# Optimization experiments

Hardware: AMD Instinct MI355X
Metric: run time of the kernel (lower is better)

The kernel has to match this reference:

```python
import jax, jax.numpy as jnp
import numpy as np

DIM = 192
STATE = 64
B = 8
H = 64
W = 64
EPS_LN = 1e-5
EPS_BN = 1e-5


def _layernorm(x, g, b):
    m = jnp.mean(x, axis=-1, keepdims=True)
    v = jnp.mean((x - m) ** 2, axis=-1, keepdims=True)
    return (x - m) / jnp.sqrt(v + EPS_LN) * g + b


def _linear(x, w, b=None):
    # torch Linear convention: w is [out, in]
    y = jnp.einsum('...i,oi->...o', x, w)
    return y if b is None else y + b


def _parallel_scan(A, Bd, xp):
    # A, Bd, xp: [B, L, S]; h_t = A_t*h_{t-1} + Bd_t*xp_t via log-space cumsum
    A_safe = jnp.clip(A, 0.001, 0.999)
    log_A = jnp.log(A_safe + 1e-10)
    log_cum_A = jnp.cumsum(log_A, axis=1)
    log_cum_A_max = jnp.max(log_cum_A, axis=1, keepdims=True)
    cum_A = jnp.exp(log_cum_A - log_cum_A_max)
    BX = Bd * xp
    # prepend zeros, drop last: normalizer uses cumprod up to t-1
    log_pad = jnp.pad(log_cum_A - log_cum_A_max, ((0, 0), (1, 0), (0, 0)))[:, :-1]
    BX_norm = BX * jnp.exp(-log_pad)
    return jnp.cumsum(BX_norm, axis=1) * cum_A


def _ssm(x, ln_g, ln_b, xp_w, xp_b, dt_w, dt_b, A_log, B_w, C_w, Dp, out_w, out_b):
    xn = _layernorm(x, ln_g, ln_b)
    delta = jax.nn.softplus(_linear(xn, dt_w, dt_b)) * 0.01 + 0.0001  # [B,L,S]
    B_t = _linear(xn, B_w)
    C_t = _linear(xn, C_w)
    A = -jnp.exp(A_log)  # [S]
    x_proj = _linear(xn, xp_w, xp_b)
    deltaA = jnp.clip(delta * A, -10.0, -0.0001)
    A_disc = jnp.exp(deltaA)
    B_disc = delta * B_t
    h = _parallel_scan(A_disc, B_disc, x_proj)
    y = C_t * h
    y = jnp.where(jnp.all(jnp.isfinite(y)), y, jnp.zeros_like(y))
    y = _linear(y, out_w, out_b)
    return y + jnp.clip(Dp, -2.0, 2.0) * x


def reference(x, ln1_g, ln1_b, ln2_g, ln2_b, dw_w, bn_g, bn_b, bn_rm, bn_rv,
              ssm_ln_g, ssm_ln_b, xp_w, xp_b, dt_w, dt_b, A_log, B_w, C_w,
              D_param, out_w, out_b, mlp_w1, mlp_b1, mlp_w2, mlp_b2,
              alpha_local, alpha_ssm, alpha_mlp):
    identity = x
    # depthwise 3x3 conv + BatchNorm2d (eval mode, running stats)
    xc = jax.lax.conv_general_dilated(
        x, dw_w, (1, 1), 'SAME', feature_group_count=DIM,
        dimension_numbers=('NCHW', 'OIHW', 'NCHW'))
    scale = (bn_g / jnp.sqrt(bn_rv + EPS_BN))[None, :, None, None]
    x_local = (xc - bn_rm[None, :, None, None]) * scale + bn_b[None, :, None, None]
    # SSM branch on flattened spatial sequence
    x_seq = x.transpose(0, 2, 3, 1).reshape(B, H * W, DIM)
    x_seq = _layernorm(x_seq, ln1_g, ln1_b)
    x_seq = _ssm(x_seq, ssm_ln_g, ssm_ln_b, xp_w, xp_b, dt_w, dt_b, A_log,
                 B_w, C_w, D_param, out_w, out_b)
    x_ssm = x_seq.reshape(B, H, W, DIM).transpose(0, 3, 1, 2)
    xr = identity + alpha_local * x_local + alpha_ssm * x_ssm
    # residual MLP (dropout = identity at inference)
    x_mlp = xr.transpose(0, 2, 3, 1).reshape(B, H * W, DIM)
    x_mlp = _layernorm(x_mlp, ln2_g, ln2_b)
    x_mlp = _linear(jax.nn.gelu(_linear(x_mlp, mlp_w1, mlp_b1), approximate=False),
                    mlp_w2, mlp_b2)
    return xr + alpha_mlp * x_mlp.reshape(B, H, W, DIM).transpose(0, 3, 1, 2)


def setup_inputs() -> dict:
    key = jax.random.key(0)
    ks = jax.random.split(key, 12)
    def nrm(k, shape, s):
        return jax.random.normal(k, shape, jnp.float32) * s
    f32 = jnp.float32
    return {
        'x': jax.random.normal(ks[0], (B, DIM, H, W), f32),
        'ln1_g': jnp.ones(DIM, f32), 'ln1_b': jnp.zeros(DIM, f32),
        'ln2_g': jnp.ones(DIM, f32), 'ln2_b': jnp.zeros(DIM, f32),
        'dw_w': nrm(ks[1], (DIM, 1, 3, 3), 0.2),
        'bn_g': jnp.ones(DIM, f32), 'bn_b': jnp.zeros(DIM, f32),
        'bn_rm': jnp.zeros(DIM, f32), 'bn_rv': jnp.ones(DIM, f32),
        'ssm_ln_g': jnp.ones(DIM, f32), 'ssm_ln_b': jnp.zeros(DIM, f32),
        'xp_w': nrm(ks[2], (STATE, DIM), 0.05), 'xp_b': jnp.zeros(STATE, f32),
        'dt_w': nrm(ks[3], (STATE, DIM), 0.05), 'dt_b': jnp.zeros(STATE, f32),
        'A_log': jnp.log(jax.random.uniform(ks[4], (STATE,), f32) * 0.8 + 0.2),
        'B_w': nrm(ks[5], (STATE, DIM), 0.05),
        'C_w': nrm(ks[6], (STATE, DIM), 0.05),
        'D_param': jnp.zeros(DIM, f32),
        'out_w': nrm(ks[7], (DIM, STATE), 0.05), 'out_b': jnp.zeros(DIM, f32),
        'mlp_w1': nrm(ks[8], (4 * DIM, DIM), 0.03), 'mlp_b1': jnp.zeros(4 * DIM, f32),
        'mlp_w2': nrm(ks[9], (DIM, 4 * DIM), 0.03), 'mlp_b2': jnp.zeros(DIM, f32),
        'alpha_local': jnp.full((1,), 0.5, f32),
        'alpha_ssm': jnp.full((1,), 0.5, f32),
        'alpha_mlp': jnp.full((1,), 0.5, f32),
    }
```

## Files before the change

kernel.cpp:

```cpp
#include <hip/hip_runtime.h>
#include <hip/hip_bf16.h>
#include <math.h>


#define DEV static __device__ __forceinline__

constexpr int Bn = 8, Dm = 192, Ln = 4096, Sn = 64, Hd = 768;

typedef __attribute__((ext_vector_type(8))) short bf16x8;
typedef __attribute__((ext_vector_type(4))) float f32x4;

DEV float wave_sum(float v) {
#pragma unroll
  for (int off = 1; off < 64; off <<= 1) v += __shfl_xor(v, off);
  return v;
}

DEV short f2b(float x) {
  __hip_bfloat16 h = __float2bfloat16(x);
  return *(short*)&h;
}

DEV float b2f(short x) {
  __hip_bfloat16 h = *(__hip_bfloat16*)&x;
  return __bfloat162float(h);
}

__global__ __launch_bounds__(256) void k_ln(
    const float* __restrict__ x, const float* __restrict__ g1, const float* __restrict__ b1,
    const float* __restrict__ g2, const float* __restrict__ b2,
    short* __restrict__ xnb, short* __restrict__ xln1b) {
  __shared__ __align__(16) float tile[Dm * 65];
  int b = blockIdx.y, l0 = blockIdx.x * 64, tid = threadIdx.x;
  const float* xb = x + (size_t)b * Dm * Ln;
  for (int i = tid; i < Dm * 16; i += 256) {
    int d = i >> 4, l4 = (i & 15) << 2;
    float4 v = *(const float4*)&xb[d * Ln + l0 + l4];
    tile[d * 65 + l4]     = v.x; tile[d * 65 + l4 + 1] = v.y;
    tile[d * 65 + l4 + 2] = v.z; tile[d * 65 + l4 + 3] = v.w;
  }
  __syncthreads();
  int lane = tid & 63, wv = tid >> 6;
  float ga0 = g1[lane], ga1 = g1[lane + 64], ga2 = g1[lane + 128];
  float bb0 = b1[lane], bb1 = b1[lane + 64], bb2 = b1[lane + 128];
  float gc0 = g2[lane], gc1 = g2[lane + 64], gc2 = g2[lane + 128];
  float bc0 = b2[lane], bc1 = b2[lane + 64], bc2 = b2[lane + 128];
  for (int li = wv; li < 64; li += 4) {
    float v0 = tile[lane * 65 + li], v1 = tile[(lane + 64) * 65 + li], v2 = tile[(lane + 128) * 65 + li];
    float s  = wave_sum(v0 + v1 + v2);
    float sq = wave_sum(v0 * v0 + v1 * v1 + v2 * v2);
    float m = s * (1.f / 192.f);
    float inv = rsqrtf(sq * (1.f / 192.f) - m * m + 1e-5f);
    float y0 = (v0 - m) * inv * ga0 + bb0;
    float y1 = (v1 - m) * inv * ga1 + bb1;
    float y2 = (v2 - m) * inv * ga2 + bb2;
    float s2  = wave_sum(y0 + y1 + y2);
    float sq2 = wave_sum(y0 * y0 + y1 * y1 + y2 * y2);
    float m2 = s2 * (1.f / 192.f);
    float inv2 = rsqrtf(sq2 * (1.f / 192.f) - m2 * m2 + 1e-5f);
    size_t base = ((size_t)b * Ln + l0 + li) * Dm;
    xln1b[base + lane]       = f2b(y0);
    xln1b[base + lane + 64]  = f2b(y1);
    xln1b[base + lane + 128] = f2b(y2);
    xnb[base + lane]       = f2b((y0 - m2) * inv2 * gc0 + bc0);
    xnb[base + lane + 64]  = f2b((y1 - m2) * inv2 * gc1 + bc1);
    xnb[base + lane + 128] = f2b((y2 - m2) * inv2 * gc2 + bc2);
  }
}

__global__ __launch_bounds__(256) void k_wconv(
    const float* __restrict__ dt_w, const float* __restrict__ B_w,
    const float* __restrict__ C_w, const float* __restrict__ xp_w,
    const float* __restrict__ out_w, const float* __restrict__ w1,
    const float* __restrict__ w2, short* __restrict__ wb) {
  int i = blockIdx.x * 256 + threadIdx.x;
  const float4* src;
  if (i < 3072)       src = (const float4*)dt_w + i;
  else if (i < 6144)  src = (const float4*)B_w + (i - 3072);
  else if (i < 9216)  src = (const float4*)C_w + (i - 6144);
  else if (i < 12288) src = (const float4*)xp_w + (i - 9216);
  else if (i < 15360) src = (const float4*)out_w + (i - 12288);
  else if (i < 52224) src = (const float4*)w1 + (i - 15360);
  else                src = (const float4*)w2 + (i - 52224);
  float4 v = *src;
  int o = i * 4;
  wb[o]     = f2b(v.x); wb[o + 1] = f2b(v.y);
  wb[o + 2] = f2b(v.z); wb[o + 3] = f2b(v.w);
}

__global__ __launch_bounds__(256) void k_proj(
    const short* __restrict__ xnb, const short* __restrict__ wcat,
    const float* __restrict__ dt_b, const float* __restrict__ xp_b,
    const float* __restrict__ A_log, float* __restrict__ abc) {
  __shared__ __align__(16) short As[64 * 72];
  __shared__ __align__(16) short Bs[256 * 72];
  int m0 = blockIdx.x * 64, tid = threadIdx.x;
  int lane = tid & 63, l16 = lane & 15, quad = lane >> 4, w = tid >> 6;
  f32x4 acc[16] = {};
  for (int kt = 0; kt < 3; kt++) {
    int kb = kt * 64;
    for (int i = tid; i < 512; i += 256) {
      int row = i >> 3, c8 = (i & 7) * 8;
      *(float4*)&As[row * 72 + c8] = *(const float4*)&xnb[(size_t)(m0 + row) * 192 + kb + c8];
    }
    for (int i = tid; i < 2048; i += 256) {
      int row = i >> 3, c8 = (i & 7) * 8;
      *(float4*)&Bs[row * 72 + c8] = *(const float4*)&wcat[(size_t)row * 192 + kb + c8];
    }
    __syncthreads();
#pragma unroll
    for (int ks = 0; ks < 2; ks++) {
      int ko = ks * 32 + quad * 8;
      bf16x8 a0 = *(const bf16x8*)&As[(w * 16 + l16) * 72 + ko];
#pragma unroll
      for (int nh = 0; nh < 2; nh++) {
        bf16x8 bfr[8];
#pragma unroll
        for (int j = 0; j < 8; j++) bfr[j] = *(const bf16x8*)&Bs[((nh * 8 + j) * 16 + l16) * 72 + ko];
#pragma unroll
        for (int j = 0; j < 8; j++)
          acc[nh * 8 + j] = __builtin_amdgcn_mfma_f32_16x16x32_bf16(a0, bfr[j], acc[nh * 8 + j], 0, 0, 0);
      }
    }
    __syncthreads();
  }
  float Av[4], dtb[4], xpb[4];
#pragma unroll
  for (int ni = 0; ni < 4; ni++) {
    int s = ni * 16 + l16;
    Av[ni] = -expf(A_log[s]); dtb[ni] = dt_b[s]; xpb[ni] = xp_b[s];
  }
#pragma unroll
  for (int r = 0; r < 4; r++) {
    int m = m0 + w * 16 + quad * 4 + r;
    float* orow = abc + (size_t)m * 192;
#pragma unroll
    for (int ni = 0; ni < 4; ni++) {
      int s = ni * 16 + l16;
      float z = acc[ni][r] + dtb[ni];
      float sp = (z > 20.f) ? z : log1pf(expf(z));
      float delta = sp * 0.01f + 0.0001f;
      float bt  = acc[ni + 4][r];
      float ct  = acc[ni + 8][r];
      float xpv = acc[ni + 12][r] + xpb[ni];
      float dA = fminf(fmaxf(delta * Av[ni], -10.f), -0.0001f);
      float Ae = fminf(fmaxf(expf(dA), 0.001f), 0.999f) + 1e-10f;
      orow[s]       = Ae;
      orow[64 + s]  = delta * bt * xpv;
      orow[128 + s] = ct;
    }
  }
}

__global__ __launch_bounds__(64) void k_scan1(const float* __restrict__ abc, float* __restrict__ sums) {
  int c = blockIdx.x, b = blockIdx.y, s = threadIdx.x;
  const float* p = abc + ((size_t)b * Ln + c * 32) * 192;
  float prodA = 1.f, h = 0.f;
  int t = 0;
  if (c == 0) { prodA = p[s]; h = p[64 + s]; t = 1; }
#pragma unroll 4
  for (; t < 32; t++) {
    float a = p[t * 192 + s], bx = p[t * 192 + 64 + s];
    h = a * (h + bx);
    prodA *= a;
  }
  int ci = b * 128 + c;
  sums[(ci * 2 + 0) * 64 + s] = prodA;
  sums[(ci * 2 + 1) * 64 + s] = h;
}

__global__ __launch_bounds__(64) void k_scan2(const float* __restrict__ sums, float* __restrict__ carries) {
  int b = blockIdx.x, s = threadIdx.x;
  float cur = 0.f;
#pragma unroll 4
  for (int c = 0; c < 128; c++) {
    int ci = b * 128 + c;
    carries[ci * 64 + s] = cur;
    cur = sums[(ci * 2 + 0) * 64 + s] * cur + sums[(ci * 2 + 1) * 64 + s];
  }
}

__global__ __launch_bounds__(64) void k_scan3(const float* __restrict__ abc, const float* __restrict__ carries,
                                              short* __restrict__ y) {
  int c = blockIdx.x, b = blockIdx.y, s = threadIdx.x;
  size_t r0 = (size_t)b * Ln + c * 32;
  const float* p = abc + r0 * 192;
  short* yo = y + r0 * 64;
  float h = carries[(b * 128 + c) * 64 + s];
  int t = 0;
  if (c == 0) { h = p[64 + s]; yo[s] = f2b(p[128 + s] * h); t = 1; }
#pragma unroll 4
  for (; t < 32; t++) {
    float a = p[t * 192 + s], bx = p[t * 192 + 64 + s], ct = p[t * 192 + 128 + s];
    h = a * (h + bx);
    yo[t * 64 + s] = f2b(ct * h);
  }
}

__global__ __launch_bounds__(256) void k_out(
    const short* __restrict__ y, const short* __restrict__ owb, const float* __restrict__ out_b,
    const float* __restrict__ Dp, const short* __restrict__ xln1b, float* __restrict__ sout) {
  __shared__ __align__(16) short As[96 * 72];
  __shared__ __align__(16) short Bs[64 * 72];
  int l0g = blockIdx.x * 64, d0 = blockIdx.y * 96, tid = threadIdx.x;
  int lane = tid & 63, l16 = lane & 15, quad = lane >> 4;
  int wm = (tid >> 6) >> 1, wn = (tid >> 6) & 1;
  f32x4 acc[3][2] = {};
  for (int i = tid; i < 768; i += 256) {
    int row = i >> 3, c8 = (i & 7) * 8;
    *(float4*)&As[row * 72 + c8] = *(const float4*)&owb[(d0 + row) * 64 + c8];
  }
  for (int i = tid; i < 512; i += 256) {
    int row = i >> 3, c8 = (i & 7) * 8;
    *(float4*)&Bs[row * 72 + c8] = *(const float4*)&y[(size_t)(l0g + row) * 64 + c8];
  }
  __syncthreads();
#pragma unroll
  for (int ks = 0; ks < 2; ks++) {
    int ko = ks * 32 + quad * 8;
    bf16x8 a[3], b[2];
#pragma unroll
    for (int mi = 0; mi < 3; mi++) a[mi] = *(const bf16x8*)&As[(wm * 48 + mi * 16 + l16) * 72 + ko];
#pragma unroll
    for (int ni = 0; ni < 2; ni++) b[ni] = *(const bf16x8*)&Bs[(wn * 32 + ni * 16 + l16) * 72 + ko];
#pragma unroll
    for (int mi = 0; mi < 3; mi++)
#pragma unroll
      for (int ni = 0; ni < 2; ni++)
        acc[mi][ni] = __builtin_amdgcn_mfma_f32_16x16x32_bf16(a[mi], b[ni], acc[mi][ni], 0, 0, 0);
  }
  int bb = l0g >> 12;
#pragma unroll
  for (int mi = 0; mi < 3; mi++)
#pragma unroll
    for (int r = 0; r < 4; r++) {
      int d = d0 + wm * 48 + mi * 16 + quad * 4 + r;
      float ob = out_b[d];
      float dc = fminf(fmaxf(Dp[d], -2.f), 2.f);
#pragma unroll
      for (int ni = 0; ni < 2; ni++) {
        int l = l0g + wn * 32 + ni * 16 + l16;
        float v = acc[mi][ni][r] + ob;
        if (dc != 0.f) v += dc * b2f(xln1b[(size_t)l * 192 + d]);
        sout[((size_t)bb * Dm + d) * Ln + (l & 4095)] = v;
      }
    }
}

__global__ __launch_bounds__(256) void k_conv(
    const float* __restrict__ x, const float* __restrict__ dw,
    const float* __restrict__ bn_g, const float* __restrict__ bn_b,
    const float* __restrict__ bn_rm, const float* __restrict__ bn_rv,
    const float* __restrict__ sout, const float* __restrict__ a_loc,
    const float* __restrict__ a_ssm, float* __restrict__ xr) {
  __shared__ __align__(16) float xs[64 * 64];
  int d = blockIdx.x, b = blockIdx.y, tid = threadIdx.x;
  const float* xp = x + ((size_t)b * Dm + d) * Ln;
  for (int i = tid; i < 1024; i += 256) ((float4*)xs)[i] = ((const float4*)xp)[i];
  __syncthreads();
  float w[9];
#pragma unroll
  for (int k = 0; k < 9; k++) w[k] = dw[d * 9 + k];
  float scale = bn_g[d] * rsqrtf(bn_rv[d] + 1e-5f);
  float rm = bn_rm[d], bb = bn_b[d];
  float al = a_loc[0], as_ = a_ssm[0];
  const float* sp = sout + ((size_t)b * Dm + d) * Ln;
  float* xo = xr + ((size_t)b * Dm + d) * Ln;
  for (int i = tid; i < 4096; i += 256) {
    int h = i >> 6, wc = i & 63;
    float acc = 0.f;
#pragma unroll
    for (int kh = 0; kh < 3; kh++) {
      int hh = h + kh - 1;
      if (hh < 0 || hh >= 64) continue;
#pragma unroll
      for (int kw = 0; kw < 3; kw++) {
        int ww2 = wc + kw - 1;
        if (ww2 < 0 || ww2 >= 64) continue;
        acc += xs[hh * 64 + ww2] * w[kh * 3 + kw];
      }
    }
    float xl = (acc - rm) * scale + bb;
    xo[i] = xs[i] + al * xl + as_ * sp[i];
  }
}

__global__ __launch_bounds__(256) void k_ln2(
    const float* __restrict__ xr, const float* __restrict__ g, const float* __restrict__ bb,
    short* __restrict__ xn2) {
  __shared__ __align__(16) float tile[Dm * 65];
  int b = blockIdx.y, l0 = blockIdx.x * 64, tid = threadIdx.x;
  const float* xb = xr + (size_t)b * Dm * Ln;
  for (int i = tid; i < Dm * 16; i += 256) {
    int d = i >> 4, l4 = (i & 15) << 2;
    float4 v = *(const float4*)&xb[d * Ln + l0 + l4];
    tile[d * 65 + l4]     = v.x; tile[d * 65 + l4 + 1] = v.y;
    tile[d * 65 + l4 + 2] = v.z; tile[d * 65 + l4 + 3] = v.w;
  }
  __syncthreads();
  int lane = tid & 63, wv = tid >> 6;
  float g0 = g[lane], g1v = g[lane + 64], g2v = g[lane + 128];
  float b0 = bb[lane], b1v = bb[lane + 64], b2v = bb[lane + 128];
  for (int li = wv; li < 64; li += 4) {
    float v0 = tile[lane * 65 + li], v1 = tile[(lane + 64) * 65 + li], v2 = tile[(lane + 128) * 65 + li];
    float s  = wave_sum(v0 + v1 + v2);
    float sq = wave_sum(v0 * v0 + v1 * v1 + v2 * v2);
    float m = s * (1.f / 192.f);
    float inv = rsqrtf(sq * (1.f / 192.f) - m * m + 1e-5f);
    size_t base = ((size_t)b * Ln + l0 + li) * Dm;
    xn2[base + lane]       = f2b((v0 - m) * inv * g0 + b0);
    xn2[base + lane + 64]  = f2b((v1 - m) * inv * g1v + b1v);
    xn2[base + lane + 128] = f2b((v2 - m) * inv * g2v + b2v);
  }
}

__global__ __launch_bounds__(256) void k_gemm1(
    const short* __restrict__ xn2, const short* __restrict__ w1b,
    const float* __restrict__ b1h, short* __restrict__ hid) {
  __shared__ __align__(16) short smem[2 * 128 * 88];
  short* As = smem;
  short* Bs = smem + 128 * 88;
  int m0 = blockIdx.x * 128, n0 = blockIdx.y * 128, tid = threadIdx.x;
  int lane = tid & 63, l16 = lane & 15, quad = lane >> 4;
  int wm = (tid >> 6) >> 1, wn = (tid >> 6) & 1;
  f32x4 acc[4][4] = {};
  for (int kt = 0; kt < 3; kt++) {
    int kb = kt * 64;
    for (int i = tid; i < 1024; i += 256) {
      int row = i >> 3, c8 = (i & 7) * 8;
      *(float4*)&As[row * 88 + c8] = *(const float4*)&xn2[(size_t)(m0 + row) * 192 + kb + c8];
      *(float4*)&Bs[row * 88 + c8] = *(const float4*)&w1b[(size_t)(n0 + row) * 192 + kb + c8];
    }
    __syncthreads();
#pragma unroll
    for (int ks = 0; ks < 2; ks++) {
      int ko = ks * 32 + quad * 8;
      bf16x8 a[4], b[4];
#pragma unroll
      for (int mi = 0; mi < 4; mi++) a[mi] = *(const bf16x8*)&As[(wm * 64 + mi * 16 + l16) * 88 + ko];
#pragma unroll
      for (int ni = 0; ni < 4; ni++) b[ni] = *(const bf16x8*)&Bs[(wn * 64 + ni * 16 + l16) * 88 + ko];
#pragma unroll
      for (int mi = 0; mi < 4; mi++)
#pragma unroll
        for (int ni = 0; ni < 4; ni++)
          acc[mi][ni] = __builtin_amdgcn_mfma_f32_16x16x32_bf16(a[mi], b[ni], acc[mi][ni], 0, 0, 0);
    }
    __syncthreads();
  }
  short* Cs = smem;
  float bias4[4];
#pragma unroll
  for (int ni = 0; ni < 4; ni++) bias4[ni] = b1h[n0 + wn * 64 + ni * 16 + l16];
#pragma unroll
  for (int mi = 0; mi < 4; mi++)
#pragma unroll
    for (int ni = 0; ni < 4; ni++) {
      int n = wn * 64 + ni * 16 + l16;
#pragma unroll
      for (int r = 0; r < 4; r++) {
        int m = wm * 64 + mi * 16 + quad * 4 + r;
        float v = acc[mi][ni][r] + bias4[ni];
        float g = 0.5f * v * (1.f + erff(v * 0.70710678118f));
        Cs[m * 136 + n] = f2b(g);
      }
    }
  __syncthreads();
  for (int i = tid; i < 2048; i += 256) {
    int m = i >> 4, ch = i & 15;
    *(float4*)&hid[(size_t)(m0 + m) * 768 + n0 + ch * 8] = *(const float4*)&Cs[m * 136 + ch * 8];
  }
}

__global__ __launch_bounds__(256) void k_gemm2(
    const short* __restrict__ hid, const short* __restrict__ w2b,
    const float* __restrict__ b2o, const float* __restrict__ xr,
    const float* __restrict__ am, float* __restrict__ out) {
  __shared__ __align__(16) short Wt[96 * 88];
  __shared__ __align__(16) short Ht[64 * 88];
  int l0g = blockIdx.x * 64, d0 = blockIdx.y * 96, tid = threadIdx.x;
  int lane = tid & 63, l16 = lane & 15, quad = lane >> 4;
  int wm = (tid >> 6) >> 1, wn = (tid >> 6) & 1;
  f32x4 acc[3][2] = {};
  for (int kt = 0; kt < 12; kt++) {
    int kb = kt * 64;
    for (int i = tid; i < 768; i += 256) {
      int row = i >> 3, c8 = (i & 7) * 8;
      *(float4*)&Wt[row * 88 + c8] = *(const float4*)&w2b[(size_t)(d0 + row) * 768 + kb + c8];
    }
    for (int i = tid; i < 512; i += 256) {
      int row = i >> 3, c8 = (i & 7) * 8;
      *(float4*)&Ht[row * 88 + c8] = *(const float4*)&hid[(size_t)(l0g + row) * 768 + kb + c8];
    }
    __syncthreads();
#pragma unroll
    for (int ks = 0; ks < 2; ks++) {
      int ko = ks * 32 + quad * 8;
      bf16x8 a[3], b[2];
#pragma unroll
      for (int mi = 0; mi < 3; mi++) a[mi] = *(const bf16x8*)&Wt[(wm * 48 + mi * 16 + l16) * 88 + ko];
#pragma unroll
      for (int ni = 0; ni < 2; ni++) b[ni] = *(const bf16x8*)&Ht[(wn * 32 + ni * 16 + l16) * 88 + ko];
#pragma unroll
      for (int mi = 0; mi < 3; mi++)
#pragma unroll
        for (int ni = 0; ni < 2; ni++)
          acc[mi][ni] = __builtin_amdgcn_mfma_f32_16x16x32_bf16(a[mi], b[ni], acc[mi][ni], 0, 0, 0);
    }
    __syncthreads();
  }
  float alpha = am[0];
#pragma unroll
  for (int mi = 0; mi < 3; mi++)
#pragma unroll
    for (int r = 0; r < 4; r++) {
      int d = d0 + wm * 48 + mi * 16 + quad * 4 + r;
      float bias = b2o[d];
#pragma unroll
      for (int ni = 0; ni < 2; ni++) {
        int lg = l0g + wn * 32 + ni * 16 + l16;
        size_t idx = ((size_t)(lg >> 12) * Dm + d) * Ln + (lg & 4095);
        out[idx] = xr[idx] + alpha * (acc[mi][ni][r] + bias);
      }
    }
}

extern "C" void kernel_launch(void* const* d_in, const int* in_sizes, int n_in,
                              void* d_out, int out_size, void* d_ws, size_t ws_size,
                              hipStream_t stream) {
  (void)in_sizes; (void)n_in; (void)out_size; (void)ws_size;
  const float* x     = (const float*)d_in[0];
  const float* ln1_g = (const float*)d_in[1];
  const float* ln1_b = (const float*)d_in[2];
  const float* ln2_g = (const float*)d_in[3];
  const float* ln2_b = (const float*)d_in[4];
  const float* dw_w  = (const float*)d_in[5];
  const float* bn_g  = (const float*)d_in[6];
  const float* bn_b  = (const float*)d_in[7];
  const float* bn_rm = (const float*)d_in[8];
  const float* bn_rv = (const float*)d_in[9];
  const float* ssm_g = (const float*)d_in[10];
  const float* ssm_b = (const float*)d_in[11];
  const float* xp_w  = (const float*)d_in[12];
  const float* xp_b  = (const float*)d_in[13];
  const float* dt_w  = (const float*)d_in[14];
  const float* dt_b  = (const float*)d_in[15];
  const float* A_log = (const float*)d_in[16];
  const float* B_w   = (const float*)d_in[17];
  const float* C_w   = (const float*)d_in[18];
  const float* Dp    = (const float*)d_in[19];
  const float* out_w = (const float*)d_in[20];
  const float* out_b = (const float*)d_in[21];
  const float* w1    = (const float*)d_in[22];
  const float* b1    = (const float*)d_in[23];
  const float* w2    = (const float*)d_in[24];
  const float* b2    = (const float*)d_in[25];
  const float* a_loc = (const float*)d_in[26];
  const float* a_ssm = (const float*)d_in[27];
  const float* a_mlp = (const float*)d_in[28];

  float* ws = (float*)d_ws;
  short* xnb   = (short*)ws;
  short* xln1b = (short*)(ws + 3145728);
  float* abc   = ws + 6291456;
  short* yB    = (short*)(ws + 12582912);
  float* sout  = ws + 13729792;
  float* xr    = ws + 20021248;
  short* wb    = (short*)(ws + 26312704);
  float* sums  = ws + 26490880;
  float* carr  = ws + 26621952;
  short* wcatb = wb;
  short* owb   = wb + 49152;
  short* w1b   = wb + 61440;
  short* w2b   = wb + 208896;
  short* xn2   = (short*)ws;
  short* hid   = (short*)(ws + 6291456);
  float* out   = (float*)d_out;

  k_ln   <<<dim3(64, 8),  256, 0, stream>>>(x, ln1_g, ln1_b, ssm_g, ssm_b, xnb, xln1b);
  k_wconv<<<dim3(348),    256, 0, stream>>>(dt_w, B_w, C_w, xp_w, out_w, w1, w2, wb);
  k_proj <<<dim3(512),    256, 0, stream>>>(xnb, wcatb, dt_b, xp_b, A_log, abc);
  k_scan1<<<dim3(128, 8),  64, 0, stream>>>(abc, sums);
  k_scan2<<<dim3(8),       64, 0, stream>>>(sums, carr);
  k_scan3<<<dim3(128, 8),  64, 0, stream>>>(abc, carr, yB);
  k_out  <<<dim3(512, 2), 256, 0, stream>>>(yB, owb, out_b, Dp, xln1b, sout);
  k_conv <<<dim3(192, 8), 256, 0, stream>>>(x, dw_w, bn_g, bn_b, bn_rm, bn_rv, sout, a_loc, a_ssm, xr);
  k_ln2  <<<dim3(64, 8),  256, 0, stream>>>(xr, ln2_g, ln2_b, xn2);
  k_gemm1<<<dim3(256, 6), 256, 0, stream>>>(xn2, w1b, b1, hid);
  k_gemm2<<<dim3(512, 2), 256, 0, stream>>>(hid, w2b, b2, xr, a_mlp, out);
}
```

Before: 294.8 us.

## Fuse weight conversion into layernorm kernel and pack scan inputs as bf16

Merges the weight-to-bf16 conversion into the layernorm kernel as an extra grid row, removing one launch. Splits the interleaved fp32 A/BX/C scan buffer into a fp32 A array and a packed pair of bf16 BX and C values, cutting the scan's read traffic from 12 to 8 bytes per element. This lowers the precision of BX and C used in the recurrence, which adds some rounding error. The workspace layout is also reshuffled so the xn2 and hid buffers no longer alias earlier ones.

```diff
diff --git a/kernel.cpp b/kernel.cpp
--- a/kernel.cpp
+++ b/kernel.cpp
@@ -26,12 +26,33 @@
   return __bfloat162float(h);
 }
 
-__global__ __launch_bounds__(256) void k_ln(
+__global__ __launch_bounds__(256) void k_prep(
     const float* __restrict__ x, const float* __restrict__ g1, const float* __restrict__ b1,
     const float* __restrict__ g2, const float* __restrict__ b2,
-    short* __restrict__ xnb, short* __restrict__ xln1b) {
+    short* __restrict__ xnb, short* __restrict__ xln1b,
+    const float* __restrict__ dt_w, const float* __restrict__ B_w,
+    const float* __restrict__ C_w, const float* __restrict__ xp_w,
+    const float* __restrict__ out_w, const float* __restrict__ w1,
+    const float* __restrict__ w2, short* __restrict__ wb) {
   __shared__ __align__(16) float tile[Dm * 65];
-  int b = blockIdx.y, l0 = blockIdx.x * 64, tid = threadIdx.x;
+  int tid = threadIdx.x;
+  if (blockIdx.y == 8) {
+    for (int i = blockIdx.x * 256 + tid; i < 89088; i += 64 * 256) {
+      const float4* src;
+      if (i < 3072)       src = (const float4*)dt_w + i;
+      else if (i < 6144)  src = (const float4*)B_w + (i - 3072);
+      else if (i < 9216)  src = (const float4*)C_w + (i - 6144);
+      else if (i < 12288) src = (const float4*)xp_w + (i - 9216);
+      else if (i < 15360) src = (const float4*)out_w + (i - 12288);
+      else if (i < 52224) src = (const float4*)w1 + (i - 15360);
+      else                src = (const float4*)w2 + (i - 52224);
+      float4 v = *src;
+      int o = i * 4;
+      wb[o] = f2b(v.x); wb[o + 1] = f2b(v.y); wb[o + 2] = f2b(v.z); wb[o + 3] = f2b(v.w);
+    }
+    return;
+  }
+  int b = blockIdx.y, l0 = blockIdx.x * 64;
   const float* xb = x + (size_t)b * Dm * Ln;
   for (int i = tid; i < Dm * 16; i += 256) {
     int d = i >> 4, l4 = (i & 15) << 2;
@@ -68,30 +89,10 @@
   }
 }
 
-__global__ __launch_bounds__(256) void k_wconv(
-    const float* __restrict__ dt_w, const float* __restrict__ B_w,
-    const float* __restrict__ C_w, const float* __restrict__ xp_w,
-    const float* __restrict__ out_w, const float* __restrict__ w1,
-    const float* __restrict__ w2, short* __restrict__ wb) {
-  int i = blockIdx.x * 256 + threadIdx.x;
-  const float4* src;
-  if (i < 3072)       src = (const float4*)dt_w + i;
-  else if (i < 6144)  src = (const float4*)B_w + (i - 3072);
-  else if (i < 9216)  src = (const float4*)C_w + (i - 6144);
-  else if (i < 12288) src = (const float4*)xp_w + (i - 9216);
-  else if (i < 15360) src = (const float4*)out_w + (i - 12288);
-  else if (i < 52224) src = (const float4*)w1 + (i - 15360);
-  else                src = (const float4*)w2 + (i - 52224);
-  float4 v = *src;
-  int o = i * 4;
-  wb[o]     = f2b(v.x); wb[o + 1] = f2b(v.y);
-  wb[o + 2] = f2b(v.z); wb[o + 3] = f2b(v.w);
-}
-
 __global__ __launch_bounds__(256) void k_proj(
     const short* __restrict__ xnb, const short* __restrict__ wcat,
     const float* __restrict__ dt_b, const float* __restrict__ xp_b,
-    const float* __restrict__ A_log, float* __restrict__ abc) {
+    const float* __restrict__ A_log, float* __restrict__ aA, unsigned* __restrict__ bxc) {
   __shared__ __align__(16) short As[64 * 72];
   __shared__ __align__(16) short Bs[256 * 72];
   int m0 = blockIdx.x * 64, tid = threadIdx.x;
@@ -124,43 +125,48 @@
     }
     __syncthreads();
   }
-  float Av[4], dtb[4], xpb[4];
+  float Av[4], dtbv[4], xpbv[4];
 #pragma unroll
   for (int ni = 0; ni < 4; ni++) {
     int s = ni * 16 + l16;
-    Av[ni] = -expf(A_log[s]); dtb[ni] = dt_b[s]; xpb[ni] = xp_b[s];
+    Av[ni] = -expf(A_log[s]); dtbv[ni] = dt_b[s]; xpbv[ni] = xp_b[s];
   }
 #pragma unroll
   for (int r = 0; r < 4; r++) {
     int m = m0 + w * 16 + quad * 4 + r;
-    float* orow = abc + (size_t)m * 192;
 #pragma unroll
     for (int ni = 0; ni < 4; ni++) {
       int s = ni * 16 + l16;
-      float z = acc[ni][r] + dtb[ni];
+      float z = acc[ni][r] + dtbv[ni];
       float sp = (z > 20.f) ? z : log1pf(expf(z));
       float delta = sp * 0.01f + 0.0001f;
       float bt  = acc[ni + 4][r];
       float ct  = acc[ni + 8][r];
-      float xpv = acc[ni + 12][r] + xpb[ni];
+      float xpv = acc[ni + 12][r] + xpbv[ni];
       float dA = fminf(fmaxf(delta * Av[ni], -10.f), -0.0001f);
       float Ae = fminf(fmaxf(expf(dA), 0.001f), 0.999f) + 1e-10f;
-      orow[s]       = Ae;
-      orow[64 + s]  = delta * bt * xpv;
-      orow[128 + s] = ct;
-    }
-  }
-}
-
-__global__ __launch_bounds__(64) void k_scan1(const float* __restrict__ abc, float* __restrict__ sums) {
+      aA[(size_t)m * 64 + s] = Ae;
+      unsigned pk = (unsigned)(unsigned short)f2b(delta * bt * xpv)
+                  | ((unsigned)(unsigned short)f2b(ct) << 16);
+      bxc[(size_t)m * 64 + s] = pk;
+    }
+  }
+}
+
+__global__ __launch_bounds__(64) void k_scan1(const float* __restrict__ aA,
+                                              const unsigned* __restrict__ bxc,
+                                              float* __restrict__ sums) {
   int c = blockIdx.x, b = blockIdx.y, s = threadIdx.x;
-  const float* p = abc + ((size_t)b * Ln + c * 32) * 192;
+  size_t r0 = (size_t)b * Ln + c * 32;
+  const float* ap = aA + r0 * 64;
+  const unsigned* bp = bxc + r0 * 64;
   float prodA = 1.f, h = 0.f;
   int t = 0;
-  if (c == 0) { prodA = p[s]; h = p[64 + s]; t = 1; }
+  if (c == 0) { prodA = ap[s]; h = b2f((short)(bp[s] & 0xFFFF)); t = 1; }
 #pragma unroll 4
   for (; t < 32; t++) {
-    float a = p[t * 192 + s], bx = p[t * 192 + 64 + s];
+    float a = ap[t * 64 + s];
+    float bx = b2f((short)(bp[t * 64 + s] & 0xFFFF));
     h = a * (h + bx);
     prodA *= a;
   }
@@ -180,20 +186,29 @@
   }
 }
 
-__global__ __launch_bounds__(64) void k_scan3(const float* __restrict__ abc, const float* __restrict__ carries,
+__global__ __launch_bounds__(64) void k_scan3(const float* __restrict__ aA,
+                                              const unsigned* __restrict__ bxc,
+                                              const float* __restrict__ carries,
                                               short* __restrict__ y) {
   int c = blockIdx.x, b = blockIdx.y, s = threadIdx.x;
   size_t r0 = (size_t)b * Ln + c * 32;
-  const float* p = abc + r0 * 192;
+  const float* ap = aA + r0 * 64;
+  const unsigned* bp = bxc + r0 * 64;
   short* yo = y + r0 * 64;
   float h = carries[(b * 128 + c) * 64 + s];
   int t = 0;
-  if (c == 0) { h = p[64 + s]; yo[s] = f2b(p[128 + s] * h); t = 1; }
+  if (c == 0) {
+    unsigned u = bp[s];
+    h = b2f((short)(u & 0xFFFF));
+    yo[s] = f2b(b2f((short)(u >> 16)) * h);
+    t = 1;
+  }
 #pragma unroll 4
   for (; t < 32; t++) {
-    float a = p[t * 192 + s], bx = p[t * 192 + 64 + s], ct = p[t * 192 + 128 + s];
-    h = a * (h + bx);
-    yo[t * 64 + s] = f2b(ct * h);
+    unsigned u = bp[t * 64 + s];
+    float a = ap[t * 64 + s];
+    h = a * (h + b2f((short)(u & 0xFFFF)));
+    yo[t * 64 + s] = f2b(b2f((short)(u >> 16)) * h);
   }
 }
 
@@ -460,29 +475,30 @@
   const float* a_mlp = (const float*)d_in[28];
 
   float* ws = (float*)d_ws;
-  short* xnb   = (short*)ws;
-  short* xln1b = (short*)(ws + 3145728);
-  float* abc   = ws + 6291456;
-  short* yB    = (short*)(ws + 12582912);
-  float* sout  = ws + 13729792;
-  float* xr    = ws + 20021248;
-  short* wb    = (short*)(ws + 26312704);
-  float* sums  = ws + 26490880;
-  float* carr  = ws + 26621952;
-  short* wcatb = wb;
-  short* owb   = wb + 49152;
-  short* w1b   = wb + 61440;
-  short* w2b   = wb + 208896;
-  short* xn2   = (short*)ws;
-  short* hid   = (short*)(ws + 6291456);
-  float* out   = (float*)d_out;
-
-  k_ln   <<<dim3(64, 8),  256, 0, stream>>>(x, ln1_g, ln1_b, ssm_g, ssm_b, xnb, xln1b);
-  k_wconv<<<dim3(348),    256, 0, stream>>>(dt_w, B_w, C_w, xp_w, out_w, w1, w2, wb);
-  k_proj <<<dim3(512),    256, 0, stream>>>(xnb, wcatb, dt_b, xp_b, A_log, abc);
-  k_scan1<<<dim3(128, 8),  64, 0, stream>>>(abc, sums);
+  short*    xnb   = (short*)ws;
+  short*    xln1b = (short*)(ws + 3145728);
+  float*    aA    = ws + 6291456;
+  unsigned* bxc   = (unsigned*)(ws + 8388608);
+  short*    yB    = (short*)(ws + 10485760);
+  float*    sout  = ws + 11534336;
+  float*    xr    = ws + 17825792;
+  short*    wb    = (short*)(ws + 24117248);
+  float*    sums  = ws + 24829952;
+  float*    carr  = ws + 24961024;
+  short*    xn2   = (short*)(ws + 25026560);
+  short*    hid   = (short*)(ws + 28172288);
+  short*    wcatb = wb;
+  short*    owb   = wb + 49152;
+  short*    w1b   = wb + 61440;
+  short*    w2b   = wb + 208896;
+  float*    out   = (float*)d_out;
+
+  k_prep <<<dim3(64, 9),  256, 0, stream>>>(x, ln1_g, ln1_b, ssm_g, ssm_b, xnb, xln1b,
+                                            dt_w, B_w, C_w, xp_w, out_w, w1, w2, wb);
+  k_proj <<<dim3(512),    256, 0, stream>>>(xnb, wcatb, dt_b, xp_b, A_log, aA, bxc);
+  k_scan1<<<dim3(128, 8),  64, 0, stream>>>(aA, bxc, sums);
   k_scan2<<<dim3(8),       64, 0, stream>>>(sums, carr);
-  k_scan3<<<dim3(128, 8),  64, 0, stream>>>(abc, carr, yB);
+  k_scan3<<<dim3(128, 8),  64, 0, stream>>>(aA, bxc, carr, yB);
   k_out  <<<dim3(512, 2), 256, 0, stream>>>(yB, owb, out_b, Dp, xln1b, sout);
   k_conv <<<dim3(192, 8), 256, 0, stream>>>(x, dw_w, bn_g, bn_b, bn_rm, bn_rv, sout, a_loc, a_ssm, xr);
   k_ln2  <<<dim3(64, 8),  256, 0, stream>>>(xr, ln2_g, ln2_b, xn2);
```

Result: no change. 290.2 us (-1.6%).
